# Optimization experiments

Measured on AMD Instinct MI355X. Metric: run time of the kernel, lower is better.

Reference implementation:

```python
import jax, jax.numpy as jnp
import numpy as np

B, N, C = 8, 4096, 512

def setup_inputs() -> dict:
    key = jax.random.key(0)
    k1, k2, k3, k4, k5, k6 = jax.random.split(key, 6)
    x = jax.random.normal(k1, (B, N, C), dtype=jnp.float32)
    adj = jax.random.uniform(k2, (B, C, C), dtype=jnp.float32)
    # params: stored [in, out] so y = x @ W + b (equivalent to torch Linear)
    s = 1.0 / np.sqrt(C)
    Wqkv = jax.random.uniform(k3, (C, 3 * C), dtype=jnp.float32, minval=-s, maxval=s)
    bqkv = jax.random.uniform(k4, (3 * C,), dtype=jnp.float32, minval=-s, maxval=s)
    Wo = jax.random.uniform(k5, (C, C), dtype=jnp.float32, minval=-s, maxval=s)
    bo = jax.random.uniform(k6, (C,), dtype=jnp.float32, minval=-s, maxval=s)
    return {"x": x, "adj": adj, "Wqkv": Wqkv, "bqkv": bqkv, "Wo": Wo, "bo": bo}

def reference(x, adj, Wqkv, bqkv, Wo, bo):
    # qkv projection + ReLU gating
    qkv = jnp.einsum('bnc,cd->bnd', x, Wqkv) + bqkv          # [B,N,3C]
    q, k, v = jnp.split(qkv, 3, axis=-1)                      # each [B,N,C]
    q, k, v = jax.nn.relu(q), jax.nn.relu(k), jax.nn.relu(v)
    dk = q.shape[-1]
    # channel-wise scores: q^T k over tokens -> [B,C,C]
    scores = jnp.einsum('bnc,bnd->bcd', q, k) / jnp.sqrt(jnp.float32(dk))
    attn = jax.nn.softmax(scores, axis=-1)
    attn = attn * adj                                         # post-softmax adjacency gate
    y = jnp.einsum('bnc,bcd->bnd', v, attn)                   # value.matmul(attention)
    return jnp.einsum('bnc,cd->bnd', y, Wo) + bo
```

## Files before the change

### kernel.cpp

```cpp
#include <hip/hip_runtime.h>

#define B_ 8
#define N_ 4096
#define C_ 512

typedef _Float16 f16;
typedef __attribute__((ext_vector_type(8))) _Float16 f16x8;
typedef __attribute__((ext_vector_type(4))) _Float16 f16x4;
typedef __attribute__((ext_vector_type(4))) float f32x4;

#define GLL16(gsrc, ldst)                                                      \
  __builtin_amdgcn_global_load_lds(                                            \
      (const __attribute__((address_space(1))) void*)(gsrc),                   \
      (__attribute__((address_space(3))) void*)(ldst), 16, 0, 0)

__device__ __forceinline__ int xcd_remap(int bid, int nwg) {
  return (bid & 7) * (nwg >> 3) + (bid >> 3);
}

template <int LDA2, int LDB2, int NT>
__device__ __forceinline__ void mainloop2(const char* __restrict__ Agb,
                                          const char* __restrict__ Bgb,
                                          f16* Als, f16* Bls,
                                          f32x4 (&acc)[4][4]) {
  const int tid = threadIdx.x;
  const int lane = tid & 63;
  const int wv = tid >> 6;
  const int wr = wv >> 1;
  const int wc = wv & 1;

  const int r15 = lane & 15;
  const int kc8 = (lane >> 4) << 3;
  const int swz = (r15 & 7) << 3;
  const int k0x = kc8 ^ swz;
  const int k1x = (kc8 + 32) ^ swz;
  const int awbase = (wr * 64 + r15) * 64;
  const int bwbase = (wc * 64 + r15) * 64;

  int rowl[4], colb[4];
#pragma unroll
  for (int ld = 0; ld < 4; ++ld) {
    const int doff = (ld * 256 + tid) * 16;
    rowl[ld] = doff >> 7;
    colb[ld] = (doff & 127) ^ ((rowl[ld] & 7) << 4);
  }

  auto stage = [&](int t) {
    if (t >= NT) return;
    f16* la = Als + (t & 1) * 8192 + wv * 512;
    f16* lb = Bls + (t & 1) * 8192 + wv * 512;
#pragma unroll
    for (int ld = 0; ld < 4; ++ld) {
      GLL16(Agb + (size_t)rowl[ld] * LDA2 + (size_t)t * 128 + colb[ld],
            la + ld * 2048);
      GLL16(Bgb + (size_t)rowl[ld] * LDB2 + (size_t)t * 128 + colb[ld],
            lb + ld * 2048);
    }
  };

  stage(0);
  __syncthreads();

  for (int T = 0; T < NT; ++T) {
    stage(T + 1);
    const f16* Ab = Als + (T & 1) * 8192;
    const f16* Bb = Bls + (T & 1) * 8192;
    f16x8 af[4][2], bf[4][2];
#pragma unroll
    for (int m = 0; m < 4; ++m) {
      af[m][0] = *(const f16x8*)(Ab + awbase + m * 1024 + k0x);
      af[m][1] = *(const f16x8*)(Ab + awbase + m * 1024 + k1x);
    }
#pragma unroll
    for (int n = 0; n < 4; ++n) {
      bf[n][0] = *(const f16x8*)(Bb + bwbase + n * 1024 + k0x);
      bf[n][1] = *(const f16x8*)(Bb + bwbase + n * 1024 + k1x);
    }
#pragma unroll
    for (int s = 0; s < 2; ++s)
#pragma unroll
      for (int m = 0; m < 4; ++m)
#pragma unroll
        for (int n = 0; n < 4; ++n)
          acc[m][n] = __builtin_amdgcn_mfma_f32_16x16x32_f16(
              af[m][s], bf[n][s], acc[m][n], 0, 0, 0);
    __syncthreads();
  }
}

#define ZERO_ACC(acc)                                                          \
  f32x4 acc[4][4];                                                             \
  _Pragma("unroll") for (int zi = 0; zi < 4; ++zi)                             \
      _Pragma("unroll") for (int zj = 0; zj < 4; ++zj) {                       \
    f32x4 z = {0.f, 0.f, 0.f, 0.f};                                            \
    acc[zi][zj] = z;                                                           \
  }

__global__ void __launch_bounds__(256)
    k_prep(const float* __restrict__ x, const float* __restrict__ Wqkv,
           const float* __restrict__ Wo, f16* __restrict__ x16,
           f16* __restrict__ wqkvt, f16* __restrict__ wot) {
  const int bid = blockIdx.x;
  if (bid < 16384) {
    const int i = bid * 256 + threadIdx.x;
    float4 v = ((const float4*)x)[i];
    f16x4 h = {(f16)v.x, (f16)v.y, (f16)v.z, (f16)v.w};
    ((f16x4*)x16)[i] = h;
  } else if (bid < 19456) {
    const int idx = (bid - 16384) * 256 + threadIdx.x;
    const int n = idx >> 9, c = idx & 511;
    wqkvt[idx] = (f16)Wqkv[(size_t)c * 1536 + n];
  } else {
    const int idx = (bid - 19456) * 256 + threadIdx.x;
    const int n = idx >> 9, c = idx & 511;
    wot[idx] = (f16)Wo[(size_t)c * 512 + n];
  }
}

__global__ void __launch_bounds__(256, 2)
    k_gemm_qkv(const f16* __restrict__ x16, const f16* __restrict__ wqkvt,
               const float* __restrict__ bqkv, f16* __restrict__ q_t,
               f16* __restrict__ k_t, f16* __restrict__ v16) {
  __shared__ alignas(16) f16 Als[2 * 8192];
  __shared__ alignas(16) f16 Bls[2 * 8192];
  const int l = xcd_remap(blockIdx.x, 3072);
  const int bx = l % 12;
  const int my = l / 12;
  const char* Agb = (const char*)(x16 + (size_t)my * 128 * C_);
  const char* Bgb = (const char*)(wqkvt + (size_t)bx * 128 * C_);
  ZERO_ACC(acc);
  mainloop2<C_ * 2, C_ * 2, C_ / 64>(Agb, Bgb, Als, Bls, acc);

  const int lane = threadIdx.x & 63, wv = threadIdx.x >> 6;
  const int wr = wv >> 1, wc = wv & 1;
  const int sec = bx >> 2;
  const int colbase = bx * 128 + wc * 64;
  const int rowbase = my * 128 + wr * 64;
  const int b = rowbase >> 12;
#pragma unroll
  for (int n = 0; n < 4; ++n) {
    const int col = colbase + n * 16 + (lane & 15);
    const int cch = col & 511;
    const float bias = bqkv[col];
#pragma unroll
    for (int m = 0; m < 4; ++m) {
      const int rg = rowbase + m * 16 + ((lane >> 4) << 2);
      const int nloc = rg & 4095;
      f32x4 a = acc[m][n];
      f16x4 h = {(f16)fmaxf(a[0] + bias, 0.f), (f16)fmaxf(a[1] + bias, 0.f),
                 (f16)fmaxf(a[2] + bias, 0.f), (f16)fmaxf(a[3] + bias, 0.f)};
      if (sec == 0) {
        *(f16x4*)(q_t + ((size_t)b * C_ + cch) * N_ + nloc) = h;
      } else if (sec == 1) {
        *(f16x4*)(k_t + ((size_t)b * C_ + cch) * N_ + nloc) = h;
      } else {
        f16* dst = v16 + (size_t)rg * C_ + cch;
        dst[0] = h[0];
        dst[C_] = h[1];
        dst[2 * C_] = h[2];
        dst[3 * C_] = h[3];
      }
    }
  }
}

__global__ void __launch_bounds__(256, 2)
    k_gemm_scores(const f16* __restrict__ q_t, const f16* __restrict__ k_t,
                  f16* __restrict__ spart) {
  __shared__ alignas(16) f16 Als[2 * 8192];
  __shared__ alignas(16) f16 Bls[2 * 8192];
  const int l = xcd_remap(blockIdx.x, 1024);
  const int bx = l & 3;
  const int by = (l >> 2) & 3;
  const int z = l >> 4;
  const int b = z >> 3, sp = z & 7;
  const char* Agb = (const char*)(q_t + (size_t)b * C_ * N_ +
                                  (size_t)(by * 128) * N_ + sp * 512);
  const char* Bgb = (const char*)(k_t + (size_t)b * C_ * N_ +
                                  (size_t)(bx * 128) * N_ + sp * 512);
  ZERO_ACC(acc);
  mainloop2<N_ * 2, N_ * 2, 8>(Agb, Bgb, Als, Bls, acc);

  const int lane = threadIdx.x & 63, wv = threadIdx.x >> 6;
  const int wr = wv >> 1, wc = wv & 1;
  f16* base = spart + (size_t)(sp * B_ + b) * C_ * C_;
#pragma unroll
  for (int n = 0; n < 4; ++n) {
    const int d = bx * 128 + wc * 64 + n * 16 + (lane & 15);
#pragma unroll
    for (int m = 0; m < 4; ++m) {
      const int c0 = by * 128 + wr * 64 + m * 16 + ((lane >> 4) << 2);
#pragma unroll
      for (int r = 0; r < 4; ++r)
        base[(size_t)(c0 + r) * C_ + d] = (f16)acc[m][n][r];
    }
  }
}

__global__ void __launch_bounds__(256)
    k_softmax_gate(const f16* __restrict__ spart,
                   const float* __restrict__ adj, f16* __restrict__ attn) {
  const int wv = threadIdx.x >> 6, lane = threadIdx.x & 63;
  const int row = blockIdx.x * 4 + wv;
  const size_t ro = (size_t)row * 512;
  const int off = lane * 8;

  float s[8] = {0.f, 0.f, 0.f, 0.f, 0.f, 0.f, 0.f, 0.f};
#pragma unroll
  for (int sp = 0; sp < 8; ++sp) {
    f16x8 v = *(const f16x8*)(spart + (size_t)sp * (B_ * C_ * C_) + ro + off);
#pragma unroll
    for (int i = 0; i < 8; ++i) s[i] += (float)v[i];
  }
  const float scale = 0.044194173824159216f;
  float mx = -1e30f;
#pragma unroll
  for (int i = 0; i < 8; ++i) {
    s[i] *= scale;
    mx = fmaxf(mx, s[i]);
  }
#pragma unroll
  for (int d = 32; d > 0; d >>= 1) mx = fmaxf(mx, __shfl_xor(mx, d, 64));
  float e[8], sum = 0.f;
#pragma unroll
  for (int i = 0; i < 8; ++i) {
    e[i] = __expf(s[i] - mx);
    sum += e[i];
  }
#pragma unroll
  for (int d = 32; d > 0; d >>= 1) sum += __shfl_xor(sum, d, 64);
  const float inv = 1.0f / sum;
  const float4 a0 = *(const float4*)(adj + ro + off);
  const float4 a1 = *(const float4*)(adj + ro + off + 4);
  f16x8 o;
  o[0] = (f16)(e[0] * inv * a0.x); o[1] = (f16)(e[1] * inv * a0.y);
  o[2] = (f16)(e[2] * inv * a0.z); o[3] = (f16)(e[3] * inv * a0.w);
  o[4] = (f16)(e[4] * inv * a1.x); o[5] = (f16)(e[5] * inv * a1.y);
  o[6] = (f16)(e[6] * inv * a1.z); o[7] = (f16)(e[7] * inv * a1.w);
  *(f16x8*)(attn + ro + off) = o;
}

__global__ void __launch_bounds__(256, 2)
    k_gemm_m(const f16* __restrict__ attn, const f16* __restrict__ wot,
             f16* __restrict__ mt) {
  __shared__ alignas(16) f16 Als[2 * 8192];
  __shared__ alignas(16) f16 Bls[2 * 8192];
  const int l = xcd_remap(blockIdx.x, 128);
  const int bx = l & 3;
  const int by = (l >> 2) & 3;
  const int b = l >> 4;
  const char* Agb = (const char*)(attn + (size_t)b * C_ * C_ +
                                  (size_t)(by * 128) * C_);
  const char* Bgb = (const char*)(wot + (size_t)(bx * 128) * C_);
  ZERO_ACC(acc);
  mainloop2<C_ * 2, C_ * 2, 8>(Agb, Bgb, Als, Bls, acc);

  const int lane = threadIdx.x & 63, wv = threadIdx.x >> 6;
  const int wr = wv >> 1, wc = wv & 1;
  f16* base = mt + (size_t)b * C_ * C_;
  const int colbase = bx * 128 + wc * 64;
  const int rowbase = by * 128 + wr * 64;
#pragma unroll
  for (int j = 0; j < 4; ++j) {
    const int e = colbase + j * 16 + (lane & 15);
#pragma unroll
    for (int i = 0; i < 4; ++i) {
      const int c0 = rowbase + i * 16 + ((lane >> 4) << 2);
      f32x4 a = acc[i][j];
      f16x4 h = {(f16)a[0], (f16)a[1], (f16)a[2], (f16)a[3]};
      *(f16x4*)(base + (size_t)e * C_ + c0) = h;
    }
  }
}

__global__ void __launch_bounds__(256, 2)
    k_gemm_out(const f16* __restrict__ v16, const f16* __restrict__ mt,
               const float* __restrict__ bo, float* __restrict__ out) {
  __shared__ alignas(16) f16 Als[2 * 8192];
  __shared__ alignas(16) f16 Bls[2 * 8192];
  const int l = xcd_remap(blockIdx.x, 1024);
  const int bx = l & 3;
  const int my = l >> 2;
  const int b = (my * 128) >> 12;
  const char* Agb = (const char*)(v16 + (size_t)my * 128 * C_);
  const char* Bgb = (const char*)(mt + (size_t)b * C_ * C_ +
                                  (size_t)(bx * 128) * C_);
  ZERO_ACC(acc);
  mainloop2<C_ * 2, C_ * 2, 8>(Agb, Bgb, Als, Bls, acc);

  const int lane = threadIdx.x & 63, wv = threadIdx.x >> 6;
  const int wr = wv >> 1, wc = wv & 1;
#pragma unroll
  for (int n = 0; n < 4; ++n) {
    const int e = bx * 128 + wc * 64 + n * 16 + (lane & 15);
    const float bias = bo[e];
#pragma unroll
    for (int m = 0; m < 4; ++m) {
      const int rg = my * 128 + wr * 64 + m * 16 + ((lane >> 4) << 2);
#pragma unroll
      for (int r = 0; r < 4; ++r)
        out[(size_t)(rg + r) * C_ + e] = acc[m][n][r] + bias;
    }
  }
}

extern "C" void kernel_launch(void* const* d_in, const int* in_sizes, int n_in,
                              void* d_out, int out_size, void* d_ws,
                              size_t ws_size, hipStream_t stream) {
  const float* x = (const float*)d_in[0];
  const float* adj = (const float*)d_in[1];
  const float* Wqkv = (const float*)d_in[2];
  const float* bqkv = (const float*)d_in[3];
  const float* Wo = (const float*)d_in[4];
  const float* bo = (const float*)d_in[5];
  float* out = (float*)d_out;

  char* ws = (char*)d_ws;
  size_t off = 0;
  auto carve = [&](size_t bytes) -> char* {
    char* p = ws + off;
    off += (bytes + 255) & ~(size_t)255;
    return p;
  };
  f16* x16 = (f16*)carve((size_t)B_ * N_ * C_ * 2);
  f16* wqkvt = (f16*)carve((size_t)3 * C_ * C_ * 2);
  f16* wot = (f16*)carve((size_t)C_ * C_ * 2);
  f16* q_t = (f16*)carve((size_t)B_ * C_ * N_ * 2);
  f16* k_t = (f16*)carve((size_t)B_ * C_ * N_ * 2);
  f16* v16 = (f16*)carve((size_t)B_ * N_ * C_ * 2);
  f16* spart = x16;
  f16* attn16 = k_t;
  f16* mt16 = q_t;

  k_prep<<<20480, 256, 0, stream>>>(x, Wqkv, Wo, x16, wqkvt, wot);
  k_gemm_qkv<<<3072, 256, 0, stream>>>(x16, wqkvt, bqkv, q_t, k_t, v16);
  k_gemm_scores<<<1024, 256, 0, stream>>>(q_t, k_t, spart);
  k_softmax_gate<<<1024, 256, 0, stream>>>(spart, adj, attn16);
  k_gemm_m<<<128, 256, 0, stream>>>(attn16, wot, mt16);
  k_gemm_out<<<1024, 256, 0, stream>>>(v16, mt16, bo, out);
}
```

Before: 169.9 us.

## Fuse fp32-to-fp16 conversion of x into the QKV GEMM A-tile load

Removes the separate pass that converted x to fp16 in k_prep. The QKV GEMM now loads fp32 x directly through registers, converts to fp16 and writes swizzled LDS tiles, while B keeps the async global_load_lds path. This drops a full write and re-read of a 32MB fp16 buffer. In exchange the GEMM reads twice as many A bytes per tile, reused across 12 column blocks, and adds register pressure plus synchronous loads in the main loop.

```diff
diff --git a/kernel.cpp b/kernel.cpp
--- a/kernel.cpp
+++ b/kernel.cpp
@@ -88,6 +88,110 @@
   }
 }
 
+template <int NT>
+__device__ __forceinline__ void mainloop2x(const float* __restrict__ Ag,
+                                           const char* __restrict__ Bgb,
+                                           f16* Als, f16* Bls,
+                                           f32x4 (&acc)[4][4]) {
+  const int tid = threadIdx.x;
+  const int lane = tid & 63;
+  const int wv = tid >> 6;
+  const int wr = wv >> 1;
+  const int wc = wv & 1;
+
+  const int r15 = lane & 15;
+  const int kc8 = (lane >> 4) << 3;
+  const int swz = (r15 & 7) << 3;
+  const int k0x = kc8 ^ swz;
+  const int k1x = (kc8 + 32) ^ swz;
+  const int awbase = (wr * 64 + r15) * 64;
+  const int bwbase = (wc * 64 + r15) * 64;
+
+  int rowl[4], colb[4];
+#pragma unroll
+  for (int ld = 0; ld < 4; ++ld) {
+    const int doff = (ld * 256 + tid) * 16;
+    rowl[ld] = doff >> 7;
+    colb[ld] = (doff & 127) ^ ((rowl[ld] & 7) << 4);
+  }
+  auto stageB = [&](int t) {
+    if (t >= NT) return;
+    f16* lb = Bls + (t & 1) * 8192 + wv * 512;
+#pragma unroll
+    for (int ld = 0; ld < 4; ++ld)
+      GLL16(Bgb + (size_t)rowl[ld] * (C_ * 2) + (size_t)t * 128 + colb[ld],
+            lb + ld * 2048);
+  };
+
+  int arow[4], akslot[4], awaddr[4];
+#pragma unroll
+  for (int w = 0; w < 4; ++w) {
+    const int id = w * 256 + tid;
+    arow[w] = id >> 3;
+    akslot[w] = id & 7;
+    awaddr[w] = arow[w] * 64 + (akslot[w] ^ (arow[w] & 7)) * 8;
+  }
+  auto loadA = [&](int t, float4 (&lo)[4], float4 (&hi)[4]) {
+    if (t >= NT) return;
+#pragma unroll
+    for (int w = 0; w < 4; ++w) {
+      const float* s = Ag + (size_t)arow[w] * C_ + t * 64 + akslot[w] * 8;
+      lo[w] = *(const float4*)s;
+      hi[w] = *(const float4*)(s + 4);
+    }
+  };
+  auto writeA = [&](int t, float4 (&lo)[4], float4 (&hi)[4]) {
+    if (t >= NT) return;
+    f16* la = Als + (t & 1) * 8192;
+#pragma unroll
+    for (int w = 0; w < 4; ++w) {
+      f16x8 h;
+      h[0] = (f16)lo[w].x; h[1] = (f16)lo[w].y;
+      h[2] = (f16)lo[w].z; h[3] = (f16)lo[w].w;
+      h[4] = (f16)hi[w].x; h[5] = (f16)hi[w].y;
+      h[6] = (f16)hi[w].z; h[7] = (f16)hi[w].w;
+      *(f16x8*)(la + awaddr[w]) = h;
+    }
+  };
+
+  {
+    float4 lo[4], hi[4];
+    loadA(0, lo, hi);
+    stageB(0);
+    writeA(0, lo, hi);
+  }
+  __syncthreads();
+
+  for (int T = 0; T < NT; ++T) {
+    float4 lo[4], hi[4];
+    loadA(T + 1, lo, hi);
+    stageB(T + 1);
+    const f16* Ab = Als + (T & 1) * 8192;
+    const f16* Bb = Bls + (T & 1) * 8192;
+    f16x8 af[4][2], bf[4][2];
+#pragma unroll
+    for (int m = 0; m < 4; ++m) {
+      af[m][0] = *(const f16x8*)(Ab + awbase + m * 1024 + k0x);
+      af[m][1] = *(const f16x8*)(Ab + awbase + m * 1024 + k1x);
+    }
+#pragma unroll
+    for (int n = 0; n < 4; ++n) {
+      bf[n][0] = *(const f16x8*)(Bb + bwbase + n * 1024 + k0x);
+      bf[n][1] = *(const f16x8*)(Bb + bwbase + n * 1024 + k1x);
+    }
+#pragma unroll
+    for (int s = 0; s < 2; ++s)
+#pragma unroll
+      for (int m = 0; m < 4; ++m)
+#pragma unroll
+        for (int n = 0; n < 4; ++n)
+          acc[m][n] = __builtin_amdgcn_mfma_f32_16x16x32_f16(
+              af[m][s], bf[n][s], acc[m][n], 0, 0, 0);
+    writeA(T + 1, lo, hi);
+    __syncthreads();
+  }
+}
+
 #define ZERO_ACC(acc)                                                          \
   f32x4 acc[4][4];                                                             \
   _Pragma("unroll") for (int zi = 0; zi < 4; ++zi)                             \
@@ -97,28 +201,22 @@
   }
 
 __global__ void __launch_bounds__(256)
-    k_prep(const float* __restrict__ x, const float* __restrict__ Wqkv,
-           const float* __restrict__ Wo, f16* __restrict__ x16,
+    k_prep(const float* __restrict__ Wqkv, const float* __restrict__ Wo,
            f16* __restrict__ wqkvt, f16* __restrict__ wot) {
   const int bid = blockIdx.x;
-  if (bid < 16384) {
-    const int i = bid * 256 + threadIdx.x;
-    float4 v = ((const float4*)x)[i];
-    f16x4 h = {(f16)v.x, (f16)v.y, (f16)v.z, (f16)v.w};
-    ((f16x4*)x16)[i] = h;
-  } else if (bid < 19456) {
-    const int idx = (bid - 16384) * 256 + threadIdx.x;
+  if (bid < 3072) {
+    const int idx = bid * 256 + threadIdx.x;
     const int n = idx >> 9, c = idx & 511;
     wqkvt[idx] = (f16)Wqkv[(size_t)c * 1536 + n];
   } else {
-    const int idx = (bid - 19456) * 256 + threadIdx.x;
+    const int idx = (bid - 3072) * 256 + threadIdx.x;
     const int n = idx >> 9, c = idx & 511;
     wot[idx] = (f16)Wo[(size_t)c * 512 + n];
   }
 }
 
 __global__ void __launch_bounds__(256, 2)
-    k_gemm_qkv(const f16* __restrict__ x16, const f16* __restrict__ wqkvt,
+    k_gemm_qkv(const float* __restrict__ x, const f16* __restrict__ wqkvt,
                const float* __restrict__ bqkv, f16* __restrict__ q_t,
                f16* __restrict__ k_t, f16* __restrict__ v16) {
   __shared__ alignas(16) f16 Als[2 * 8192];
@@ -126,10 +224,10 @@
   const int l = xcd_remap(blockIdx.x, 3072);
   const int bx = l % 12;
   const int my = l / 12;
-  const char* Agb = (const char*)(x16 + (size_t)my * 128 * C_);
+  const float* Ag = x + (size_t)my * 128 * C_;
   const char* Bgb = (const char*)(wqkvt + (size_t)bx * 128 * C_);
   ZERO_ACC(acc);
-  mainloop2<C_ * 2, C_ * 2, C_ / 64>(Agb, Bgb, Als, Bls, acc);
+  mainloop2x<C_ / 64>(Ag, Bgb, Als, Bls, acc);
 
   const int lane = threadIdx.x & 63, wv = threadIdx.x >> 6;
   const int wr = wv >> 1, wc = wv & 1;
@@ -322,18 +420,17 @@
     off += (bytes + 255) & ~(size_t)255;
     return p;
   };
-  f16* x16 = (f16*)carve((size_t)B_ * N_ * C_ * 2);
+  f16* spart = (f16*)carve((size_t)8 * B_ * C_ * C_ * 2);
   f16* wqkvt = (f16*)carve((size_t)3 * C_ * C_ * 2);
   f16* wot = (f16*)carve((size_t)C_ * C_ * 2);
   f16* q_t = (f16*)carve((size_t)B_ * C_ * N_ * 2);
   f16* k_t = (f16*)carve((size_t)B_ * C_ * N_ * 2);
   f16* v16 = (f16*)carve((size_t)B_ * N_ * C_ * 2);
-  f16* spart = x16;
   f16* attn16 = k_t;
   f16* mt16 = q_t;
 
-  k_prep<<<20480, 256, 0, stream>>>(x, Wqkv, Wo, x16, wqkvt, wot);
-  k_gemm_qkv<<<3072, 256, 0, stream>>>(x16, wqkvt, bqkv, q_t, k_t, v16);
+  k_prep<<<4096, 256, 0, stream>>>(Wqkv, Wo, wqkvt, wot);
+  k_gemm_qkv<<<3072, 256, 0, stream>>>(x, wqkvt, bqkv, q_t, k_t, v16);
   k_gemm_scores<<<1024, 256, 0, stream>>>(q_t, k_t, spart);
   k_softmax_gate<<<1024, 256, 0, stream>>>(spart, adj, attn16);
   k_gemm_m<<<128, 256, 0, stream>>>(attn16, wot, mt16);
```

Measured after the change: 195.7 us. 15.2% more time.
